# Optimization experiments

Hardware: AMD Instinct MI355X
Metric: run time of the kernel (lower is better)

## Reference

```python
import jax, jax.numpy as jnp
import numpy as np

B, S, D, H = 2, 2048, 2048, 16
DH = D // H  # 128


def setup_inputs() -> dict:
    key = jax.random.key(0)
    ks = jax.random.split(key, 7)
    x = jax.random.normal(ks[0], (B, S, D), dtype=jnp.float32)
    # causal mask [b, s, s], True = attend
    mask = jnp.broadcast_to(jnp.tril(jnp.ones((S, S), dtype=bool)), (B, S, S))
    scale = 1.0 / np.sqrt(D)
    Wq = jax.random.normal(ks[1], (D, H, DH), dtype=jnp.float32) * scale
    Wk = jax.random.normal(ks[2], (D, 1, DH), dtype=jnp.float32) * scale
    Wv = jax.random.normal(ks[3], (D, 1, DH), dtype=jnp.float32) * scale
    Wo = jax.random.normal(ks[4], (H, DH, D), dtype=jnp.float32) * scale
    bo = jnp.zeros((D,), dtype=jnp.float32)
    return {"x": x, "mask": mask, "Wq": Wq, "Wk": Wk, "Wv": Wv, "Wo": Wo, "bo": bo}


def reference(x, mask, Wq, Wk, Wv, Wo, bo):
    # projections: q [b,s,h,dh]; k,v [b,s,1,dh] (single shared KV head)
    q = jnp.einsum("bsd,dhe->bshe", x, Wq)
    k = jnp.einsum("bsd,dhe->bshe", x, Wk)[:, :, 0, :]  # [b,s,dh]
    v = jnp.einsum("bsd,dhe->bshe", x, Wv)[:, :, 0, :]  # [b,s,dh]
    # scores [b,h,s,s] with 1/sqrt(d_head) scaling
    scores = jnp.einsum("bqhe,bke->bhqk", q, k) / jnp.sqrt(
        jnp.asarray(q.shape[-1], dtype=q.dtype)
    )
    big_neg = jnp.finfo(scores.dtype).min
    scores = jnp.where(mask[:, None, :, :], scores, big_neg)
    probs = jax.nn.softmax(scores, axis=-1)
    attn = jnp.einsum("bhqk,bke->bhqe", probs, v)  # [b,h,s,dh]
    # output projection contracting (head, d_head) -> d_state, with bias
    out = jnp.einsum("bhqe,hed->bqd", attn, Wo) + bo
    return out
```

## Files before the change

kernel.cpp:

```cpp
#include <hip/hip_runtime.h>
#include <cmath>
#include <cstdint>

typedef __bf16 bf16;
typedef __bf16 bf16x8 __attribute__((ext_vector_type(8)));
typedef __bf16 bf16x4 __attribute__((ext_vector_type(4)));
typedef float f32x4 __attribute__((ext_vector_type(4)));

#define SDIM 2048
#define DDIM 2048
#define NQKV 2304
#define DH   128

__device__ __forceinline__ void glds16(const bf16* g, bf16* l) {
    __builtin_amdgcn_global_load_lds(
        (const __attribute__((address_space(1))) void*)g,
        (__attribute__((address_space(3))) void*)l, 16, 0, 0);
}

__global__ __launch_bounds__(256) void prep_kernel(const float* __restrict__ x,
                                                   const float* __restrict__ Wq,
                                                   const float* __restrict__ Wk,
                                                   const float* __restrict__ Wv,
                                                   const float* __restrict__ Wo,
                                                   bf16* __restrict__ xb,
                                                   bf16* __restrict__ Wqkv_t,
                                                   bf16* __restrict__ Wo_t) {
    __shared__ float tile[32][33];
    int bx = blockIdx.x;
    if (bx < 8192) {
        int i = bx * 256 + threadIdx.x;
        float4 v = reinterpret_cast<const float4*>(x)[i];
        bf16x4 o;
        o[0] = (bf16)v.x; o[1] = (bf16)v.y; o[2] = (bf16)v.z; o[3] = (bf16)v.w;
        reinterpret_cast<bf16x4*>(xb)[i] = o;
        return;
    }
    bx -= 8192;
    const float* src; bf16* dst; int srcN; int t;
    if (bx < 4096)      { src = Wq; dst = Wqkv_t;                      srcN = 2048; t = bx; }
    else if (bx < 4352) { src = Wk; dst = Wqkv_t + (size_t)2048*2048;  srcN = 128;  t = bx - 4096; }
    else if (bx < 4608) { src = Wv; dst = Wqkv_t + (size_t)2176*2048;  srcN = 128;  t = bx - 4352; }
    else                { src = Wo; dst = Wo_t;                        srcN = 2048; t = bx - 4608; }
    const int srcK = 2048;
    int ntx = srcN >> 5;
    int n0 = (t % ntx) * 32, k0 = (t / ntx) * 32;
    int tx = threadIdx.x & 31;
    int ty = threadIdx.x >> 5;
    for (int i = 0; i < 4; i++)
        tile[ty + i*8][tx] = src[(size_t)(k0 + ty + i*8) * srcN + n0 + tx];
    __syncthreads();
    for (int i = 0; i < 4; i++)
        dst[(size_t)(n0 + ty + i*8) * srcK + k0 + tx] = (bf16)tile[tx][ty + i*8];
}

__global__ __launch_bounds__(256) void vtrans_kernel(const bf16* __restrict__ QKV,
                                                     bf16* __restrict__ Vt) {
    __shared__ bf16 tile[32][33];
    int tx = threadIdx.x & 31;
    int ty = threadIdx.x >> 5;
    int d0 = blockIdx.x * 32;
    int s0 = blockIdx.y * 32;
    int b  = blockIdx.z;
    for (int i = 0; i < 4; i++)
        tile[ty + i*8][tx] = QKV[((size_t)b * SDIM + s0 + ty + i*8) * NQKV + 2176 + d0 + tx];
    __syncthreads();
    for (int i = 0; i < 4; i++)
        Vt[((size_t)b * DH + d0 + ty + i*8) * SDIM + s0 + tx] = tile[tx][ty + i*8];
}

template<int WRITE_F32>
__global__ __launch_bounds__(256) void gemm_bt_kernel(const bf16* __restrict__ A,
                                                      const bf16* __restrict__ Bt,
                                                      void* __restrict__ Cout,
                                                      const float* __restrict__ bias,
                                                      int K, int N) {
    __shared__ bf16 As[128 * 32];
    __shared__ bf16 Bs[128 * 32];
    const int tid  = threadIdx.x;
    const int wave = tid >> 6, lane = tid & 63;
    const int quad = lane >> 4, l15 = lane & 15;
    const int tm = blockIdx.x * 128, tn = blockIdx.y * 128;
    const int wm = (wave >> 1) * 64, wn = (wave & 1) * 64;

    const int lrow = lane >> 2, lcol = (lane & 3) * 8;
    const int wrow = wave * 32;
    const bf16* Ag0 = A  + (size_t)(tm + wrow + lrow)      * K + lcol;
    const bf16* Ag1 = A  + (size_t)(tm + wrow + 16 + lrow) * K + lcol;
    const bf16* Bg0 = Bt + (size_t)(tn + wrow + lrow)      * K + lcol;
    const bf16* Bg1 = Bt + (size_t)(tn + wrow + 16 + lrow) * K + lcol;
    bf16* Al0 = As + (wrow)      * 32;
    bf16* Al1 = As + (wrow + 16) * 32;
    bf16* Bl0 = Bs + (wrow)      * 32;
    bf16* Bl1 = Bs + (wrow + 16) * 32;

    f32x4 acc[4][4];
    for (int i = 0; i < 4; i++)
        for (int j = 0; j < 4; j++) acc[i][j] = (f32x4)0.0f;

    for (int k0 = 0; k0 < K; k0 += 32) {
        __syncthreads();
        glds16(Ag0 + k0, Al0);
        glds16(Ag1 + k0, Al1);
        glds16(Bg0 + k0, Bl0);
        glds16(Bg1 + k0, Bl1);
        __syncthreads();
        bf16x8 af[4], bfr[4];
        for (int i = 0; i < 4; i++)
            af[i]  = *reinterpret_cast<const bf16x8*>(As + (wm + i*16 + l15) * 32 + quad*8);
        for (int j = 0; j < 4; j++)
            bfr[j] = *reinterpret_cast<const bf16x8*>(Bs + (wn + j*16 + l15) * 32 + quad*8);
        for (int i = 0; i < 4; i++)
            for (int j = 0; j < 4; j++)
                acc[i][j] = __builtin_amdgcn_mfma_f32_16x16x32_bf16(af[i], bfr[j], acc[i][j], 0, 0, 0);
    }

    for (int i = 0; i < 4; i++)
        for (int j = 0; j < 4; j++)
            for (int r = 0; r < 4; r++) {
                int row = tm + wm + i*16 + quad*4 + r;
                int col = tn + wn + j*16 + l15;
                float v = acc[i][j][r];
                if (WRITE_F32)
                    reinterpret_cast<float*>(Cout)[(size_t)row * N + col] = v + bias[col];
                else
                    reinterpret_cast<bf16*>(Cout)[(size_t)row * N + col] = (bf16)v;
            }
}

#define FPLD 72

__global__ __launch_bounds__(512) void flash_kernel(const bf16* __restrict__ QKV,
                                                    const bf16* __restrict__ Vt,
                                                    bf16* __restrict__ attn) {
    __shared__ bf16 KVS[16384];
    __shared__ bf16 Ps[8 * 16 * FPLD];
    bf16* Ks  = KVS;
    bf16* Vts = KVS + 8192;

    const int tid  = threadIdx.x;
    const int wave = tid >> 6, lane = tid & 63;
    const int quad = lane >> 4, l15 = lane & 15;
    const int bx = blockIdx.x;
    const int qs = 255 - (bx >> 1);
    const int b  = bx & 1;
    const int q  = qs * 8 + wave;
    const size_t rowbase = (size_t)b * SDIM;
    const bf16* Vtb = Vt + (size_t)b * DH * SDIM;
    const float scale = 0.088388347648318447f;

    const int s0 = wave, s1 = wave + 8;
    const int krow0 = s0*4 + (lane >> 4), krow1 = s1*4 + (lane >> 4);
    const int kchunk = lane & 15;
    const bf16* kg0 = QKV + (rowbase + krow0) * NQKV + 2048 + ((kchunk ^ (krow0 & 15)) * 8);
    const bf16* kg1 = QKV + (rowbase + krow1) * NQKV + 2048 + ((kchunk ^ (krow1 & 15)) * 8);
    bf16* kl0 = Ks + s0 * 512;
    bf16* kl1 = Ks + s1 * 512;
    const int vrow0 = s0*8 + (lane >> 3), vrow1 = s1*8 + (lane >> 3);
    const int vchunk = lane & 7;
    const bf16* vg0 = Vtb + (size_t)vrow0 * SDIM + ((vchunk ^ (vrow0 & 7)) * 8);
    const bf16* vg1 = Vtb + (size_t)vrow1 * SDIM + ((vchunk ^ (vrow1 & 7)) * 8);
    bf16* vl0 = Vts + s0 * 512;
    bf16* vl1 = Vts + s1 * 512;

    bf16x8 qf[4];
    {
        const bf16* qp = QKV + (rowbase + q) * NQKV + l15 * DH + quad * 8;
        for (int kk = 0; kk < 4; kk++)
            qf[kk] = *reinterpret_cast<const bf16x8*>(qp + kk * 32);
    }
    float l_s[4] = {0.0f, 0.0f, 0.0f, 0.0f};
    f32x4 acc[8];
    for (int d = 0; d < 8; d++) acc[d] = (f32x4)0.0f;

    const int ntiles = (qs >> 3) + 1;
    bf16* Pw = Ps + wave * (16 * FPLD);

    const bf16* kp0 = kg0; const bf16* kp1 = kg1;
    const bf16* vp0 = vg0; const bf16* vp1 = vg1;

    for (int t = 0; t < ntiles; t++) {
        const int key0 = t * 64;
        __syncthreads();
        glds16(kp0, kl0); glds16(kp1, kl1);
        glds16(vp0, vl0); glds16(vp1, vl1);
        kp0 += 64 * NQKV; kp1 += 64 * NQKV; vp0 += 64; vp1 += 64;
        __syncthreads();

        f32x4 sc[4];
        for (int c = 0; c < 4; c++) sc[c] = (f32x4)0.0f;
        for (int c = 0; c < 4; c++)
            for (int kk = 0; kk < 4; kk++) {
                int j = (kk*4 + quad) ^ l15;
                bf16x8 kf = *reinterpret_cast<const bf16x8*>(
                    Ks + (c*16 + l15) * 128 + j * 8);
                sc[c] = __builtin_amdgcn_mfma_f32_16x16x32_bf16(qf[kk], kf, sc[c], 0, 0, 0);
            }

        const bool tail = (key0 + 63 > q);
        for (int c = 0; c < 4; c++)
            for (int r = 0; r < 4; r++) {
                float p;
                if (tail && (key0 + c*16 + l15 > q)) p = 0.0f;
                else p = __expf(sc[c][r] * scale);
                l_s[r] += p;
                Pw[(quad*4 + r) * FPLD + c*16 + l15] = (bf16)p;
            }

        for (int kk2 = 0; kk2 < 2; kk2++) {
            bf16x8 pf = *reinterpret_cast<const bf16x8*>(Pw + l15 * FPLD + kk2*32 + quad*8);
            for (int dd = 0; dd < 8; dd++) {
                int d = dd*16 + l15;
                int j = (kk2*4 + quad) ^ (l15 & 7);
                bf16x8 vf = *reinterpret_cast<const bf16x8*>(Vts + d * 64 + j * 8);
                acc[dd] = __builtin_amdgcn_mfma_f32_16x16x32_bf16(pf, vf, acc[dd], 0, 0, 0);
            }
        }
    }

    __syncthreads();

    for (int d = 1; d < 16; d <<= 1)
        for (int r = 0; r < 4; r++) l_s[r] += __shfl_xor(l_s[r], d);

    bf16* Ow = KVS + wave * 2048;
    for (int r = 0; r < 4; r++) {
        float inv = 1.0f / l_s[r];
        for (int d = 0; d < 8; d++)
            Ow[(quad*4 + r) * 128 + d*16 + l15] = (bf16)(acc[d][r] * inv);
    }
    const int orow = lane >> 2;
    const int ocol = (lane & 3) * 8;
    bf16* ob = attn + (rowbase + q) * (size_t)DDIM;
    for (int it = 0; it < 4; it++)
        *reinterpret_cast<uint4*>(ob + orow * DH + ocol + it*32) =
            *reinterpret_cast<const uint4*>(Ow + orow * 128 + ocol + it*32);
}

extern "C" void kernel_launch(void* const* d_in, const int* in_sizes, int n_in,
                              void* d_out, int out_size, void* d_ws, size_t ws_size,
                              hipStream_t stream) {
    const float* x  = (const float*)d_in[0];
    const float* Wq = (const float*)d_in[2];
    const float* Wk = (const float*)d_in[3];
    const float* Wv = (const float*)d_in[4];
    const float* Wo = (const float*)d_in[5];
    const float* bo = (const float*)d_in[6];
    float* out = (float*)d_out;

    char* ws = (char*)d_ws;
    bf16* xb     = (bf16*)(ws);
    bf16* Wqkv_t = (bf16*)(ws + 16777216);
    bf16* Wo_t   = (bf16*)(ws + 26214400);
    bf16* QKV    = (bf16*)(ws + 34603008);
    bf16* attn   = (bf16*)(ws + 53477376);
    bf16* Vtb    = (bf16*)(ws + 70254592);
    (void)ws_size; (void)in_sizes; (void)n_in; (void)out_size;

    prep_kernel<<<16896, 256, 0, stream>>>(x, Wq, Wk, Wv, Wo, xb, Wqkv_t, Wo_t);
    gemm_bt_kernel<0><<<dim3(32, 18), 256, 0, stream>>>(xb, Wqkv_t, (void*)QKV, nullptr, 2048, 2304);
    vtrans_kernel<<<dim3(4, 64, 2), 256, 0, stream>>>(QKV, Vtb);
    flash_kernel<<<512, 512, 0, stream>>>(QKV, Vtb, attn);
    gemm_bt_kernel<1><<<dim3(32, 16), 256, 0, stream>>>(attn, Wo_t, (void*)out, bo, 2048, 2048);
}
```

Measured before the change: 313.5 us.

## Replace GEMM with 256x256 tiled, double-buffered, swizzled 8-wave pipelined kernel

Swaps the simple 128x128 single-buffered GEMM for a 512-thread 256x256-tile kernel that double-buffers K=64 slices in LDS. It issues async global-to-LDS loads interleaved with MFMA phases, uses an XOR swizzle against bank conflicts, and raises MFMA priority with s_setprio. The aim is to hide load latency, raise arithmetic intensity and cut barrier stalls in the QKV and output projections. The costs are 128KB of LDS per block and fewer blocks (144 and 128), which may underfill the 256 CUs.

```diff
diff --git a/kernel.cpp b/kernel.cpp
--- a/kernel.cpp
+++ b/kernel.cpp
@@ -17,6 +17,9 @@
         (const __attribute__((address_space(1))) void*)g,
         (__attribute__((address_space(3))) void*)l, 16, 0, 0);
 }
+
+#define MEMFENCE() asm volatile("" ::: "memory")
+#define SBAR() do { MEMFENCE(); __builtin_amdgcn_s_barrier(); MEMFENCE(); } while (0)
 
 __global__ __launch_bounds__(256) void prep_kernel(const float* __restrict__ x,
                                                    const float* __restrict__ Wq,
@@ -70,57 +73,137 @@
 }
 
 template<int WRITE_F32>
-__global__ __launch_bounds__(256) void gemm_bt_kernel(const bf16* __restrict__ A,
-                                                      const bf16* __restrict__ Bt,
-                                                      void* __restrict__ Cout,
-                                                      const float* __restrict__ bias,
-                                                      int K, int N) {
-    __shared__ bf16 As[128 * 32];
-    __shared__ bf16 Bs[128 * 32];
+__global__ __launch_bounds__(512, 2) void gemm8_kernel(const bf16* __restrict__ A,
+                                                       const bf16* __restrict__ Bt,
+                                                       void* __restrict__ Cout,
+                                                       const float* __restrict__ bias,
+                                                       int N) {
+    constexpr int K  = 2048;
+    constexpr int NT = 32;
+    __shared__ bf16 smem[65536];
+
     const int tid  = threadIdx.x;
     const int wave = tid >> 6, lane = tid & 63;
     const int quad = lane >> 4, l15 = lane & 15;
-    const int tm = blockIdx.x * 128, tn = blockIdx.y * 128;
-    const int wm = (wave >> 1) * 64, wn = (wave & 1) * 64;
-
-    const int lrow = lane >> 2, lcol = (lane & 3) * 8;
-    const int wrow = wave * 32;
-    const bf16* Ag0 = A  + (size_t)(tm + wrow + lrow)      * K + lcol;
-    const bf16* Ag1 = A  + (size_t)(tm + wrow + 16 + lrow) * K + lcol;
-    const bf16* Bg0 = Bt + (size_t)(tn + wrow + lrow)      * K + lcol;
-    const bf16* Bg1 = Bt + (size_t)(tn + wrow + 16 + lrow) * K + lcol;
-    bf16* Al0 = As + (wrow)      * 32;
-    bf16* Al1 = As + (wrow + 16) * 32;
-    bf16* Bl0 = Bs + (wrow)      * 32;
-    bf16* Bl1 = Bs + (wrow + 16) * 32;
-
-    f32x4 acc[4][4];
-    for (int i = 0; i < 4; i++)
-        for (int j = 0; j < 4; j++) acc[i][j] = (f32x4)0.0f;
-
-    for (int k0 = 0; k0 < K; k0 += 32) {
-        __syncthreads();
-        glds16(Ag0 + k0, Al0);
-        glds16(Ag1 + k0, Al1);
-        glds16(Bg0 + k0, Bl0);
-        glds16(Bg1 + k0, Bl1);
-        __syncthreads();
-        bf16x8 af[4], bfr[4];
-        for (int i = 0; i < 4; i++)
-            af[i]  = *reinterpret_cast<const bf16x8*>(As + (wm + i*16 + l15) * 32 + quad*8);
-        for (int j = 0; j < 4; j++)
-            bfr[j] = *reinterpret_cast<const bf16x8*>(Bs + (wn + j*16 + l15) * 32 + quad*8);
-        for (int i = 0; i < 4; i++)
-            for (int j = 0; j < 4; j++)
-                acc[i][j] = __builtin_amdgcn_mfma_f32_16x16x32_bf16(af[i], bfr[j], acc[i][j], 0, 0, 0);
-    }
-
-    for (int i = 0; i < 4; i++)
-        for (int j = 0; j < 4; j++)
+    const int wm = wave >> 2, wn = wave & 3;
+    const int tm = blockIdx.x * 256, tn = blockIdx.y * 256;
+
+    const int r0 = wave * 32 + (lane >> 2);
+    const int cs = (lane & 3) ^ ((lane >> 3) & 3);
+    const bf16* Ag = A  + (size_t)(tm + r0) * K + cs * 8;
+    const bf16* Bg = Bt + (size_t)(tn + r0) * K + cs * 8;
+    bf16* Asl = smem + wave * 1024;
+    bf16* Bsl = smem + 32768 + wave * 1024;
+
+    auto STAGE_A = [&](int t, int kh) {
+        if (t < NT) {
+            const bf16* s = Ag + t * 64 + kh * 32;
+            bf16* d = Asl + (t & 1) * 16384 + kh * 8192;
+            glds16(s, d);
+            glds16(s + 16 * K, d + 512);
+        }
+    };
+    auto STAGE_B = [&](int t, int kh) {
+        if (t < NT) {
+            const bf16* s = Bg + t * 64 + kh * 32;
+            bf16* d = Bsl + (t & 1) * 16384 + kh * 8192;
+            glds16(s, d);
+            glds16(s + 16 * K, d + 512);
+        }
+    };
+
+    const int rsw  = (l15 >> 1) & 3;
+    const int aoff = (wm * 128 + l15) * 32 + ((quad ^ rsw) * 8);
+    const int boff = (wn * 64  + l15) * 32 + ((quad ^ rsw) * 8);
+
+    f32x4 acc[8][4];
+#pragma unroll
+    for (int m = 0; m < 8; m++)
+#pragma unroll
+        for (int n = 0; n < 4; n++) acc[m][n] = (f32x4)0.0f;
+
+    STAGE_A(0, 0); STAGE_B(0, 0);
+    STAGE_A(0, 1); STAGE_B(0, 1);
+    STAGE_A(1, 0); STAGE_B(1, 0);
+    asm volatile("s_waitcnt vmcnt(4)" ::: "memory");
+    SBAR();
+
+    bf16x8 av[4], bv[4];
+    for (int t = 0; t < NT; ++t) {
+        const int buf = t & 1;
+        const bf16* Sa = smem + buf * 16384;
+        const bf16* Sb = smem + 32768 + buf * 16384;
+
+#pragma unroll
+        for (int m = 0; m < 4; m++) av[m] = *reinterpret_cast<const bf16x8*>(Sa + aoff + m * 512);
+#pragma unroll
+        for (int n = 0; n < 4; n++) bv[n] = *reinterpret_cast<const bf16x8*>(Sb + boff + n * 512);
+        STAGE_A(t + 1, 1);
+        SBAR();
+        __builtin_amdgcn_s_setprio(1);
+#pragma unroll
+        for (int m = 0; m < 4; m++)
+#pragma unroll
+            for (int n = 0; n < 4; n++)
+                acc[m][n] = __builtin_amdgcn_mfma_f32_16x16x32_bf16(av[m], bv[n], acc[m][n], 0, 0, 0);
+        __builtin_amdgcn_s_setprio(0);
+        SBAR();
+
+#pragma unroll
+        for (int m = 0; m < 4; m++) av[m] = *reinterpret_cast<const bf16x8*>(Sa + aoff + 2048 + m * 512);
+        STAGE_B(t + 1, 1);
+        SBAR();
+        __builtin_amdgcn_s_setprio(1);
+#pragma unroll
+        for (int m = 0; m < 4; m++)
+#pragma unroll
+            for (int n = 0; n < 4; n++)
+                acc[4 + m][n] = __builtin_amdgcn_mfma_f32_16x16x32_bf16(av[m], bv[n], acc[4 + m][n], 0, 0, 0);
+        __builtin_amdgcn_s_setprio(0);
+        if (t + 1 < NT) { asm volatile("s_waitcnt vmcnt(8)" ::: "memory"); }
+        else            { asm volatile("s_waitcnt vmcnt(0)" ::: "memory"); }
+        SBAR();
+
+#pragma unroll
+        for (int m = 0; m < 4; m++) av[m] = *reinterpret_cast<const bf16x8*>(Sa + 8192 + aoff + m * 512);
+#pragma unroll
+        for (int n = 0; n < 4; n++) bv[n] = *reinterpret_cast<const bf16x8*>(Sb + 8192 + boff + n * 512);
+        STAGE_A(t + 2, 0);
+        SBAR();
+        __builtin_amdgcn_s_setprio(1);
+#pragma unroll
+        for (int m = 0; m < 4; m++)
+#pragma unroll
+            for (int n = 0; n < 4; n++)
+                acc[m][n] = __builtin_amdgcn_mfma_f32_16x16x32_bf16(av[m], bv[n], acc[m][n], 0, 0, 0);
+        __builtin_amdgcn_s_setprio(0);
+        SBAR();
+
+#pragma unroll
+        for (int m = 0; m < 4; m++) av[m] = *reinterpret_cast<const bf16x8*>(Sa + 8192 + aoff + 2048 + m * 512);
+        STAGE_B(t + 2, 0);
+        SBAR();
+        __builtin_amdgcn_s_setprio(1);
+#pragma unroll
+        for (int m = 0; m < 4; m++)
+#pragma unroll
+            for (int n = 0; n < 4; n++)
+                acc[4 + m][n] = __builtin_amdgcn_mfma_f32_16x16x32_bf16(av[m], bv[n], acc[4 + m][n], 0, 0, 0);
+        __builtin_amdgcn_s_setprio(0);
+        if (t + 2 < NT) { asm volatile("s_waitcnt vmcnt(4)" ::: "memory"); }
+        else            { asm volatile("s_waitcnt vmcnt(0)" ::: "memory"); }
+        SBAR();
+    }
+
+#pragma unroll
+    for (int m = 0; m < 8; m++)
+#pragma unroll
+        for (int n = 0; n < 4; n++)
+#pragma unroll
             for (int r = 0; r < 4; r++) {
-                int row = tm + wm + i*16 + quad*4 + r;
-                int col = tn + wn + j*16 + l15;
-                float v = acc[i][j][r];
+                int row = tm + wm * 128 + m * 16 + quad * 4 + r;
+                int col = tn + wn * 64 + n * 16 + l15;
+                float v = acc[m][n][r];
                 if (WRITE_F32)
                     reinterpret_cast<float*>(Cout)[(size_t)row * N + col] = v + bias[col];
                 else
@@ -258,8 +341,8 @@
     (void)ws_size; (void)in_sizes; (void)n_in; (void)out_size;
 
     prep_kernel<<<16896, 256, 0, stream>>>(x, Wq, Wk, Wv, Wo, xb, Wqkv_t, Wo_t);
-    gemm_bt_kernel<0><<<dim3(32, 18), 256, 0, stream>>>(xb, Wqkv_t, (void*)QKV, nullptr, 2048, 2304);
+    gemm8_kernel<0><<<dim3(16, 9), 512, 0, stream>>>(xb, Wqkv_t, (void*)QKV, nullptr, 2304);
     vtrans_kernel<<<dim3(4, 64, 2), 256, 0, stream>>>(QKV, Vtb);
     flash_kernel<<<512, 512, 0, stream>>>(QKV, Vtb, attn);
-    gemm_bt_kernel<1><<<dim3(32, 16), 256, 0, stream>>>(attn, Wo_t, (void*)out, bo, 2048, 2048);
-}
+    gemm8_kernel<1><<<dim3(16, 8), 512, 0, stream>>>(attn, Wo_t, (void*)out, bo, 2048);
+}
```

Measured after the change: 303.5 us. -3.2%, faster.
